# Optimization experiments

Measured on AMD Instinct MI355X. Metric: run time of the kernel, lower is better.

Reference implementation:

```python
import jax, jax.numpy as jnp
import numpy as np

TAU = 1.0
TOP_K = 2

def setup_inputs() -> dict:
    key = jax.random.key(0)
    ks = jax.random.split(key, 5)
    B, C, H, W, E, GH = 16, 64, 128, 128, 8, 16
    return {
        "x": jax.random.normal(ks[0], (B, C, H, W), dtype=jnp.float32),
        "wg1": jax.random.normal(ks[1], (C, GH), dtype=jnp.float32) * 0.1,
        "bg1": jnp.zeros((GH,), dtype=jnp.float32),
        "wg2": jax.random.normal(ks[2], (GH, E), dtype=jnp.float32) * 0.1,
        "bg2": jnp.zeros((E,), dtype=jnp.float32),
        "w_exp": jax.random.normal(ks[3], (E, C, C, 3, 3), dtype=jnp.float32) * 0.05,
        "b_exp": jnp.zeros((E, C), dtype=jnp.float32),
    }

def reference(x, wg1, bg1, wg2, bg2, w_exp, b_exp):
    B, C, H, W = x.shape
    E = w_exp.shape[0]
    # in_proj / out_proj are Identity (c1 == mid_channels == c2)
    x_proj = x
    # gate: GAP -> Linear -> ReLU -> Linear
    pooled = x_proj.mean(axis=(2, 3))                      # [B, C]
    h = jax.nn.relu(pooled @ wg1 + bg1)                    # [B, GH]
    gate_logits = h @ wg2 + bg2                            # [B, E]
    # soft top-k routing (hard=False)
    gate_probs = jax.nn.softmax(gate_logits / TAU, axis=-1)
    _, topk_idx = jax.lax.top_k(gate_probs, TOP_K)         # [B, K]
    mask = jnp.zeros_like(gate_probs).at[jnp.arange(B)[:, None], topk_idx].set(1.0)
    sparse_probs = gate_probs * mask
    sparse_probs = sparse_probs / (sparse_probs.sum(axis=-1, keepdims=True) + 1e-8)
    # dense all-expert 3x3 conv: fold experts into one grouped-output conv
    kern = w_exp.reshape(E * C, C, 3, 3)                   # [E*C, C, 3, 3]
    y = jax.lax.conv_general_dilated(
        x_proj, kern, window_strides=(1, 1), padding="SAME",
        dimension_numbers=("NCHW", "OIHW", "NCHW"))
    y = y.reshape(B, E, C, H, W) + b_exp[None, :, :, None, None]
    # vectorized weighted combine (replaces the per-sample python loop)
    out = jnp.einsum("be,bechw->bchw", sparse_probs, y)
    # shortcut (c1 == c2)
    return out + x
```

## Files before the change

### kernel.cpp

```cpp
#include <hip/hip_runtime.h>
#include <hip/hip_bf16.h>
#include <math.h>

#define B_  16
#define C_  64
#define HW_ 128
#define E_  8
#define GH_ 16

typedef __attribute__((ext_vector_type(8))) short short8;
typedef __attribute__((ext_vector_type(4))) float float4v;

#define ROWS_LDS 4
#define COLS_LDS 132
#define XS_SHORTS (ROWS_LDS * COLS_LDS * 32)
#define WB_PER_B (9 * 2 * 4 * 64 * 8)

__global__ __launch_bounds__(256) void pool_kernel(const float* __restrict__ x,
                                                   float* __restrict__ pooled) {
  const int bc = blockIdx.x;
  const float4v* p4 = (const float4v*)(x + (size_t)bc * (HW_ * HW_));
  float4v s4 = {0.f, 0.f, 0.f, 0.f};
  for (int i = threadIdx.x; i < (HW_ * HW_) / 4; i += 256) s4 += p4[i];
  float s = (s4.x + s4.y) + (s4.z + s4.w);
#pragma unroll
  for (int off = 32; off > 0; off >>= 1) s += __shfl_down(s, off, 64);
  __shared__ float red[4];
  if ((threadIdx.x & 63) == 0) red[threadIdx.x >> 6] = s;
  __syncthreads();
  if (threadIdx.x == 0)
    pooled[bc] = (red[0] + red[1] + red[2] + red[3]) * (1.0f / (HW_ * HW_));
}

__global__ __launch_bounds__(256) void combine_kernel(
    const float* __restrict__ w_exp, const float* __restrict__ pooled,
    const float* __restrict__ wg1, const float* __restrict__ bg1,
    const float* __restrict__ wg2, const float* __restrict__ bg2,
    const float* __restrict__ b_exp, __hip_bfloat16* __restrict__ wB,
    float* __restrict__ bcomb) {
  __shared__ float wtmp[8 * 576];
  __shared__ float hsh[GH_];
  __shared__ float psh[E_];
  const int t = threadIdx.x;
  const int b = blockIdx.x >> 3;
  const int cog = blockIdx.x & 7;

  if (t < GH_) {
    float s = bg1[t];
    for (int c = 0; c < C_; c++)
      s = fmaf(pooled[b * C_ + c], wg1[c * GH_ + t], s);
    hsh[t] = fmaxf(s, 0.f);
  }
  __syncthreads();
  if (t == 0) {
    float p[E_];
    float mx = -1e30f;
#pragma unroll
    for (int e = 0; e < E_; e++) {
      float s = bg2[e];
#pragma unroll
      for (int g = 0; g < GH_; g++) s = fmaf(hsh[g], wg2[g * E_ + e], s);
      p[e] = s;
      mx = fmaxf(mx, s);
    }
    float sum = 0.f;
#pragma unroll
    for (int e = 0; e < E_; e++) { p[e] = expf(p[e] - mx); sum += p[e]; }
    const float inv = 1.0f / sum;
#pragma unroll
    for (int e = 0; e < E_; e++) p[e] *= inv;
    int i1 = 0;
#pragma unroll
    for (int e = 1; e < E_; e++) if (p[e] > p[i1]) i1 = e;
    int i2 = -1;
#pragma unroll
    for (int e = 0; e < E_; e++) {
      if (e == i1) continue;
      if (i2 < 0 || p[e] > p[i2]) i2 = e;
    }
    const float denom = p[i1] + p[i2] + 1e-8f;
#pragma unroll
    for (int e = 0; e < E_; e++)
      psh[e] = (e == i1 || e == i2) ? (p[e] / denom) : 0.f;
  }
  __syncthreads();
  float pb[E_];
#pragma unroll
  for (int e = 0; e < E_; e++) pb[e] = psh[e];

  const size_t src0 = (size_t)cog * 8 * 576;
  for (int i = t; i < 4608; i += 256) {
    float s = 0.f;
#pragma unroll
    for (int e = 0; e < E_; e++)
      s = fmaf(pb[e], w_exp[(size_t)e * (C_ * 576) + src0 + i], s);
    wtmp[i] = s;
  }
  __syncthreads();
  for (int i = t; i < 4608; i += 256) {
    const int j = i & 7;
    const int co_l = (i >> 3) & 7;
    const int rest = i >> 6;
    const int quad = rest & 3;
    const int khalf = (rest >> 2) & 1;
    const int pos = rest >> 3;
    const int ci = khalf * 32 + quad * 8 + j;
    const int co = cog * 8 + co_l;
    float v = wtmp[co_l * 576 + ci * 9 + pos];
    if (pos == 4 && co == ci) v += 1.0f;
    wB[(size_t)b * WB_PER_B +
       ((((pos * 2 + khalf) * 4 + quad) * 64) + co) * 8 + j] =
        __float2bfloat16(v);
  }
  if (t < 8) {
    const int co = cog * 8 + t;
    float s = 0.f;
#pragma unroll
    for (int e = 0; e < E_; e++) s = fmaf(pb[e], b_exp[e * C_ + co], s);
    bcomb[b * C_ + co] = s;
  }
}

__global__ __launch_bounds__(256, 4) void conv_kernel(
    const float* __restrict__ x, const __hip_bfloat16* __restrict__ wB,
    const float* __restrict__ bcomb, float* __restrict__ out) {
  __shared__ __align__(16) short xs[XS_SHORTS];

  const int t = threadIdx.x;
  const int blk = blockIdx.x;
  const int xcd = blk & 7;
  const int idx = blk >> 3;
  const int b = xcd * 2 + (idx >> 6);
  const int strip = idx & 63;
  const int ty = strip * 2;

  const int wave = t >> 6;
  const int L = t & 63;
  const int n16 = L & 15;
  const int quad = L >> 4;

  float bias[4];
#pragma unroll
  for (int nt = 0; nt < 4; nt++) bias[nt] = bcomb[b * C_ + nt * 16 + n16];

  float4v acc[4][4];
#pragma unroll
  for (int mt = 0; mt < 4; mt++)
#pragma unroll
    for (int nt = 0; nt < 4; nt++) acc[mt][nt] = (float4v)0.f;

  for (int h = 0; h < 2; h++) {
    __syncthreads();
#pragma unroll
    for (int it = 0; it < 2; it++) {
      const int i = it * 256 + t;
      const int scq = i & 31;
      const int grp = (i >> 5) & 3;
      const int r = i >> 7;
      const int gh = ty + r - 1;
      const int ci = h * 32 + grp * 8;
      float4v v[8];
      if ((unsigned)gh < (unsigned)HW_) {
        const float* p =
            x + ((size_t)(b * C_ + ci) * HW_ + gh) * HW_ + scq * 4;
#pragma unroll
        for (int k = 0; k < 8; k++)
          v[k] = *(const float4v*)(p + (size_t)k * (HW_ * HW_));
      } else {
#pragma unroll
        for (int k = 0; k < 8; k++) v[k] = (float4v)0.f;
      }
      const int slot = grp ^ (scq & 3);
#pragma unroll
      for (int kk = 0; kk < 4; kk++) {
        const int cl = scq * 4 + kk + 1;
        short8 pk;
#pragma unroll
        for (int k = 0; k < 8; k++) {
          __hip_bfloat16 bb = __float2bfloat16(v[k][kk]);
          pk[k] = *(short*)&bb;
        }
        *(short8*)&xs[((r * COLS_LDS + cl) * 4 + slot) * 8] = pk;
      }
    }
    if (t < 32) {
      const int r = t >> 3;
      const int edge = (t >> 2) & 1;
      const int slot = t & 3;
      const int cl = edge ? 129 : 0;
      *(short8*)&xs[((r * COLS_LDS + cl) * 4 + slot) * 8] = (short8)0;
    }
    __syncthreads();

    const __hip_bfloat16* wBh =
        wB + (size_t)b * WB_PER_B + (size_t)(h * 4 + quad) * 512 + n16 * 8;
    short8 bf[2][4];
#pragma unroll
    for (int nt = 0; nt < 4; nt++)
      bf[0][nt] = *(const short8*)(wBh + nt * 128);

#pragma unroll
    for (int pos = 0; pos < 9; pos++) {
      const int cur = pos & 1;
      if (pos < 8) {
#pragma unroll
        for (int nt = 0; nt < 4; nt++)
          bf[cur ^ 1][nt] =
              *(const short8*)(wBh + (size_t)(pos + 1) * 4096 + nt * 128);
      }
      const int kh = pos / 3;
      const int kw = pos - kh * 3;
      short8 a[4];
#pragma unroll
      for (int mt = 0; mt < 4; mt++) {
        const int mtg = wave * 4 + mt;
        const int lr = (mtg >> 3) + kh;
        const int cl = (mtg & 7) * 16 + n16 + kw;
        const int slot = quad ^ (((cl - 1) >> 2) & 3);
        a[mt] = *(const short8*)&xs[((lr * COLS_LDS + cl) * 4 + slot) * 8];
      }
#pragma unroll
      for (int mt = 0; mt < 4; mt++)
#pragma unroll
        for (int nt = 0; nt < 4; nt++)
          acc[mt][nt] = __builtin_amdgcn_mfma_f32_16x16x32_bf16(
              a[mt], bf[cur][nt], acc[mt][nt], 0, 0, 0);
    }
  }

#pragma unroll
  for (int mtp = 0; mtp < 4; mtp += 2) {
#pragma unroll
    for (int nt = 0; nt < 4; nt++) {
#pragma unroll
      for (int d = 0; d < 2; d++) {
        const int mt = mtp + d;
        const int mtg = wave * 4 + mt;
        const int row = ty + (mtg >> 3);
        const int cb = (mtg & 7) * 16 + quad * 4;
        float4v o = acc[mt][nt];
        o.x += bias[nt];
        o.y += bias[nt];
        o.z += bias[nt];
        o.w += bias[nt];
        *(float4v*)(out +
                    ((size_t)(b * C_ + nt * 16 + n16) * HW_ + row) * HW_ + cb) =
            o;
      }
    }
  }
}

extern "C" void kernel_launch(void* const* d_in, const int* in_sizes, int n_in,
                              void* d_out, int out_size, void* d_ws,
                              size_t ws_size, hipStream_t stream) {
  const float* x     = (const float*)d_in[0];
  const float* wg1   = (const float*)d_in[1];
  const float* bg1   = (const float*)d_in[2];
  const float* wg2   = (const float*)d_in[3];
  const float* bg2   = (const float*)d_in[4];
  const float* w_exp = (const float*)d_in[5];
  const float* b_exp = (const float*)d_in[6];
  float* out = (float*)d_out;

  float* ws = (float*)d_ws;
  float* pooled = ws;
  float* bcomb  = ws + 1024;
  __hip_bfloat16* wB = (__hip_bfloat16*)(ws + 2048);

  pool_kernel<<<B_ * C_, 256, 0, stream>>>(x, pooled);
  combine_kernel<<<B_ * 8, 256, 0, stream>>>(w_exp, pooled, wg1, bg1, wg2, bg2,
                                             b_exp, wB, bcomb);
  conv_kernel<<<1024, 256, 0, stream>>>(x, wB, bcomb, out);
}
```

Baseline: 188.2 us.

## Pre-transpose input to NHWC bf16 fused with pooling, stage via direct LDS loads

Replaces the standalone pooling pass with a kernel that reads x once, writes a bf16 NHWC (channel-swizzled) copy into workspace and emits per-row-block partial sums. The combine kernel reduces these partials. A new conv kernel double-buffers both channel halves in LDS using global_load_lds from the bf16 copy, which removes the per-block fp32 load and convert work. Its epilogue uses lane shuffles to write wider contiguous output. The cost is an extra 32 MB bf16 write and read, plus a dependency on workspace size, with a fallback to the old path when the workspace is too small.

```diff
diff --git a/kernel.cpp b/kernel.cpp
--- a/kernel.cpp
+++ b/kernel.cpp
@@ -9,12 +9,90 @@
 #define GH_ 16
 
 typedef __attribute__((ext_vector_type(8))) short short8;
+typedef __attribute__((ext_vector_type(4))) short short4v;
 typedef __attribute__((ext_vector_type(4))) float float4v;
+
+#define WB_PER_B (9 * 2 * 4 * 64 * 8)
+
+#define WS_WB_OFF     0
+#define WS_WB_BYTES   (B_ * WB_PER_B * 2)
+#define WS_BCOMB_OFF  (WS_WB_OFF + WS_WB_BYTES)
+#define WS_BCOMB_BYTES (B_ * C_ * 4)
+#define WS_PP_OFF     (WS_BCOMB_OFF + WS_BCOMB_BYTES)
+#define WS_PP_BYTES   (B_ * C_ * 64 * 4)
+#define WS_XP_OFF     (WS_PP_OFF + WS_PP_BYTES)
+#define WS_XP_BYTES   ((size_t)B_ * HW_ * HW_ * C_ * 2)
+#define WS_NEED       ((size_t)WS_XP_OFF + WS_XP_BYTES)
 
 #define ROWS_LDS 4
 #define COLS_LDS 132
 #define XS_SHORTS (ROWS_LDS * COLS_LDS * 32)
-#define WB_PER_B (9 * 2 * 4 * 64 * 8)
+
+#define COLS_V2 130
+#define BUF_SHORTS (4 * COLS_V2 * 32)
+
+__global__ __launch_bounds__(256) void transpose_pool_kernel(
+    const float* __restrict__ x, __hip_bfloat16* __restrict__ xp,
+    float* __restrict__ pp) {
+  __shared__ float pred[256 * 4];
+  const int t = threadIdx.x;
+  const int b = blockIdx.x >> 6;
+  const int rb = blockIdx.x & 63;
+  const int cg = t & 15;
+  const int cq = t >> 4;
+  const int g = cg >> 1;
+  const int kh = g >> 2;
+  const int g_lo = g & 3;
+  const int h4 = cg & 1;
+
+  float s0 = 0.f, s1 = 0.f, s2 = 0.f, s3 = 0.f;
+
+  for (int rr = 0; rr < 2; rr++) {
+    const int r = rb * 2 + rr;
+    const float* xr = x + ((size_t)b * C_ * HW_ + (size_t)r) * HW_;
+    __hip_bfloat16* xpr = xp + ((size_t)(b * HW_ + r) * HW_) * C_;
+#pragma unroll
+    for (int ih = 0; ih < 2; ih++) {
+      const int w4 = ih * 16 + cq;
+      float4v v0 = *(const float4v*)(xr + (size_t)(cg * 4 + 0) * (HW_ * HW_) + w4 * 4);
+      float4v v1 = *(const float4v*)(xr + (size_t)(cg * 4 + 1) * (HW_ * HW_) + w4 * 4);
+      float4v v2 = *(const float4v*)(xr + (size_t)(cg * 4 + 2) * (HW_ * HW_) + w4 * 4);
+      float4v v3 = *(const float4v*)(xr + (size_t)(cg * 4 + 3) * (HW_ * HW_) + w4 * 4);
+      s0 += (v0.x + v0.y) + (v0.z + v0.w);
+      s1 += (v1.x + v1.y) + (v1.z + v1.w);
+      s2 += (v2.x + v2.y) + (v2.z + v2.w);
+      s3 += (v3.x + v3.y) + (v3.z + v3.w);
+      const int pos_lo = g_lo ^ (w4 & 3);
+      const int coff = kh * 32 + pos_lo * 8 + h4 * 4;
+#pragma unroll
+      for (int j = 0; j < 4; j++) {
+        const int w = w4 * 4 + j;
+        __hip_bfloat16 b0 = __float2bfloat16(v0[j]);
+        __hip_bfloat16 b1 = __float2bfloat16(v1[j]);
+        __hip_bfloat16 b2 = __float2bfloat16(v2[j]);
+        __hip_bfloat16 b3 = __float2bfloat16(v3[j]);
+        short4v pk;
+        pk[0] = *(short*)&b0;
+        pk[1] = *(short*)&b1;
+        pk[2] = *(short*)&b2;
+        pk[3] = *(short*)&b3;
+        *(short4v*)(xpr + (size_t)w * C_ + coff) = pk;
+      }
+    }
+  }
+  pred[t * 4 + 0] = s0;
+  pred[t * 4 + 1] = s1;
+  pred[t * 4 + 2] = s2;
+  pred[t * 4 + 3] = s3;
+  __syncthreads();
+  if (t < C_) {
+    const int kk = t & 3, cgr = t >> 2;
+    float a = 0.f;
+#pragma unroll
+    for (int m = 0; m < 16; m++) a += pred[(cgr + 16 * m) * 4 + kk];
+    pp[((size_t)b * C_ + t) * 64 + rb] = a;
+  }
+}
 
 __global__ __launch_bounds__(256) void pool_kernel(const float* __restrict__ x,
                                                    float* __restrict__ pooled) {
@@ -34,6 +112,7 @@
 
 __global__ __launch_bounds__(256) void combine_kernel(
     const float* __restrict__ w_exp, const float* __restrict__ pooled,
+    const float* __restrict__ pp, const int use_pp,
     const float* __restrict__ wg1, const float* __restrict__ bg1,
     const float* __restrict__ wg2, const float* __restrict__ bg2,
     const float* __restrict__ b_exp, __hip_bfloat16* __restrict__ wB,
@@ -41,14 +120,28 @@
   __shared__ float wtmp[8 * 576];
   __shared__ float hsh[GH_];
   __shared__ float psh[E_];
+  __shared__ float pool_sh[C_];
   const int t = threadIdx.x;
   const int b = blockIdx.x >> 3;
   const int cog = blockIdx.x & 7;
 
+  if (use_pp) {
+    if (t < C_) {
+      const float4v* pr = (const float4v*)(pp + ((size_t)b * C_ + t) * 64);
+      float4v s4 = {0.f, 0.f, 0.f, 0.f};
+#pragma unroll
+      for (int m = 0; m < 16; m++) s4 += pr[m];
+      pool_sh[t] = ((s4.x + s4.y) + (s4.z + s4.w)) * (1.0f / (HW_ * HW_));
+    }
+  } else {
+    if (t < C_) pool_sh[t] = pooled[b * C_ + t];
+  }
+  __syncthreads();
+
   if (t < GH_) {
     float s = bg1[t];
     for (int c = 0; c < C_; c++)
-      s = fmaf(pooled[b * C_ + c], wg1[c * GH_ + t], s);
+      s = fmaf(pool_sh[c], wg1[c * GH_ + t], s);
     hsh[t] = fmaxf(s, 0.f);
   }
   __syncthreads();
@@ -121,7 +214,142 @@
   }
 }
 
-__global__ __launch_bounds__(256, 4) void conv_kernel(
+__device__ __forceinline__ float4v shx1(float4v v) {
+  float4v r;
+  r.x = __shfl_xor(v.x, 1, 64);
+  r.y = __shfl_xor(v.y, 1, 64);
+  r.z = __shfl_xor(v.z, 1, 64);
+  r.w = __shfl_xor(v.w, 1, 64);
+  return r;
+}
+
+__global__ __launch_bounds__(256, 2) void conv_kernel_v2(
+    const __hip_bfloat16* __restrict__ xp, const __hip_bfloat16* __restrict__ wB,
+    const float* __restrict__ bcomb, float* __restrict__ out) {
+  __shared__ __align__(16) short xs[2][BUF_SHORTS];
+
+  const int t = threadIdx.x;
+  const int blk = blockIdx.x;
+  const int xcd = blk & 7;
+  const int idx = blk >> 3;
+  const int b = xcd * 2 + (idx >> 6);
+  const int strip = idx & 63;
+  const int ty = strip * 2;
+
+  const int wave = t >> 6;
+  const int L = t & 63;
+  const int n16 = L & 15;
+  const int quad = L >> 4;
+
+  if (t < 64) {
+    const int buf = t >> 5;
+    const int r = (t >> 3) & 3;
+    const int edge = (t >> 2) & 1;
+    const int slot = t & 3;
+    const int cl = edge ? (COLS_V2 - 1) : 0;
+    *(short8*)&xs[buf][((r * COLS_V2 + cl) * 4 + slot) * 8] = (short8)0;
+  }
+
+  float bias[4];
+#pragma unroll
+  for (int nt = 0; nt < 4; nt++) bias[nt] = bcomb[b * C_ + nt * 16 + n16];
+
+  float4v acc[4][4];
+#pragma unroll
+  for (int mt = 0; mt < 4; mt++)
+#pragma unroll
+    for (int nt = 0; nt < 4; nt++) acc[mt][nt] = (float4v)0.f;
+
+  auto stage = [&](int khs, int buf) {
+#pragma unroll
+    for (int it = 0; it < 8; it++) {
+      const int i = it * 256 + t;
+      const int slot = i & 3;
+      const int pix = i >> 2;
+      const int w = pix & 127;
+      const int r = pix >> 7;
+      const int gh = ty + r - 1;
+      short* dst = &xs[buf][((r * COLS_V2 + w + 1) * 4 + slot) * 8];
+      if ((unsigned)gh < (unsigned)HW_) {
+        const __hip_bfloat16* src =
+            xp + ((size_t)(b * HW_ + gh) * HW_ + w) * C_ + khs * 32 + slot * 8;
+        __builtin_amdgcn_global_load_lds(
+            (const __attribute__((address_space(1))) void*)src,
+            (__attribute__((address_space(3))) void*)dst, 16, 0, 0);
+      } else {
+        *(short8*)dst = (short8)0;
+      }
+    }
+  };
+
+  stage(0, 0);
+
+  for (int kh = 0; kh < 2; kh++) {
+    __syncthreads();
+    if (kh == 0) stage(1, 1);
+
+    const __hip_bfloat16* wBh =
+        wB + (size_t)b * WB_PER_B + (size_t)(kh * 4 + quad) * 512 + n16 * 8;
+    short8 bf[2][4];
+#pragma unroll
+    for (int nt = 0; nt < 4; nt++)
+      bf[0][nt] = *(const short8*)(wBh + nt * 128);
+
+#pragma unroll
+    for (int pos = 0; pos < 9; pos++) {
+      const int cur = pos & 1;
+      if (pos < 8) {
+#pragma unroll
+        for (int nt = 0; nt < 4; nt++)
+          bf[cur ^ 1][nt] =
+              *(const short8*)(wBh + (size_t)(pos + 1) * 4096 + nt * 128);
+      }
+      const int krow = pos / 3;
+      const int kw = pos - krow * 3;
+      short8 a[4];
+#pragma unroll
+      for (int mt = 0; mt < 4; mt++) {
+        const int mtg = wave * 4 + mt;
+        const int lr = (mtg >> 3) + krow;
+        const int cl = (mtg & 7) * 16 + n16 + kw;
+        const int slot = quad ^ (((cl + 127) >> 2) & 3);
+        a[mt] = *(const short8*)&xs[kh][((lr * COLS_V2 + cl) * 4 + slot) * 8];
+      }
+#pragma unroll
+      for (int mt = 0; mt < 4; mt++)
+#pragma unroll
+        for (int nt = 0; nt < 4; nt++)
+          acc[mt][nt] = __builtin_amdgcn_mfma_f32_16x16x32_bf16(
+              a[mt], bf[cur][nt], acc[mt][nt], 0, 0, 0);
+    }
+  }
+
+#pragma unroll
+  for (int mtp = 0; mtp < 4; mtp += 2) {
+    const int mtg0 = wave * 4 + mtp;
+    const int row = ty + (mtg0 >> 3);
+    const int ct0 = mtg0 & 7;
+#pragma unroll
+    for (int nt = 0; nt < 4; nt++) {
+      float4v o0 = acc[mtp][nt];
+      float4v o1 = acc[mtp + 1][nt];
+      o0 += bias[nt];
+      o1 += bias[nt];
+      const float4v vA = shx1(o1);
+      const float4v vB = shx1(o0);
+      const int odd = n16 & 1;
+      const int colb = (ct0 + odd) * 16 + quad * 4;
+      const float4v dA = odd ? vA : o0;
+      const float4v dB = odd ? o1 : vB;
+      const int chA = nt * 16 + (n16 & ~1);
+      const int chB = nt * 16 + (n16 | 1);
+      *(float4v*)(out + ((size_t)(b * C_ + chA) * HW_ + row) * HW_ + colb) = dA;
+      *(float4v*)(out + ((size_t)(b * C_ + chB) * HW_ + row) * HW_ + colb) = dB;
+    }
+  }
+}
+
+__global__ __launch_bounds__(256, 4) void conv_kernel_f32(
     const float* __restrict__ x, const __hip_bfloat16* __restrict__ wB,
     const float* __restrict__ bcomb, float* __restrict__ out) {
   __shared__ __align__(16) short xs[XS_SHORTS];
@@ -263,13 +491,22 @@
   const float* b_exp = (const float*)d_in[6];
   float* out = (float*)d_out;
 
-  float* ws = (float*)d_ws;
-  float* pooled = ws;
-  float* bcomb  = ws + 1024;
-  __hip_bfloat16* wB = (__hip_bfloat16*)(ws + 2048);
-
-  pool_kernel<<<B_ * C_, 256, 0, stream>>>(x, pooled);
-  combine_kernel<<<B_ * 8, 256, 0, stream>>>(w_exp, pooled, wg1, bg1, wg2, bg2,
-                                             b_exp, wB, bcomb);
-  conv_kernel<<<1024, 256, 0, stream>>>(x, wB, bcomb, out);
-}
+  char* ws = (char*)d_ws;
+  __hip_bfloat16* wB = (__hip_bfloat16*)(ws + WS_WB_OFF);
+  float* bcomb = (float*)(ws + WS_BCOMB_OFF);
+  float* pp    = (float*)(ws + WS_PP_OFF);
+
+  if (ws_size >= WS_NEED) {
+    __hip_bfloat16* xp = (__hip_bfloat16*)(ws + WS_XP_OFF);
+    transpose_pool_kernel<<<B_ * 64, 256, 0, stream>>>(x, xp, pp);
+    combine_kernel<<<B_ * 8, 256, 0, stream>>>(w_exp, nullptr, pp, 1, wg1, bg1,
+                                               wg2, bg2, b_exp, wB, bcomb);
+    conv_kernel_v2<<<1024, 256, 0, stream>>>(xp, wB, bcomb, out);
+  } else {
+    float* pooled = pp;
+    pool_kernel<<<B_ * C_, 256, 0, stream>>>(x, pooled);
+    combine_kernel<<<B_ * 8, 256, 0, stream>>>(w_exp, pooled, nullptr, 0, wg1,
+                                               bg1, wg2, bg2, b_exp, wB, bcomb);
+    conv_kernel_f32<<<1024, 256, 0, stream>>>(x, wB, bcomb, out);
+  }
+}
```

After: 161.3 us. -14.3%, faster.
